# Optimization experiments

Measured on AMD Instinct MI355X. Metric: run time of the kernel, lower is better.

The kernel has to match this reference:

```python
import jax, jax.numpy as jnp
import numpy as np

B, N, D, H, DH, E, BIAS_DIM = 8, 512, 512, 8, 64, 32768, 8

def setup_inputs() -> dict:
    key = jax.random.key(0)
    ks = jax.random.split(key, 10)
    states = jax.random.normal(ks[0], (B, N, D), jnp.float32)
    key_states = jax.random.normal(ks[1], (B, N, D), jnp.float32)
    # causal mask, broadcastable over heads: [B,1,N,N]
    masks = jnp.broadcast_to(jnp.tril(jnp.ones((N, N), jnp.float32)), (B, 1, N, N))
    edge_type = jax.random.randint(ks[2], (E, 1), 0, BIAS_DIM, jnp.int32)
    b_idx = jax.random.randint(ks[3], (E, 1), 0, B, jnp.int32)
    q_idx = jax.random.randint(ks[4], (E, 1), 0, N, jnp.int32)
    k_idx = jax.random.randint(ks[5], (E, 1), 0, N, jnp.int32)
    attention_bias = jnp.concatenate([edge_type, b_idx, q_idx, k_idx], axis=1)
    s = 0.05
    Wq = jax.random.normal(ks[6], (D, H, DH), jnp.float32) * s
    Wk = jax.random.normal(ks[7], (D, H, DH), jnp.float32) * s
    Wv = jax.random.normal(ks[8], (D, H, DH), jnp.float32) * s
    k2 = jax.random.split(ks[9], 3)
    Wo = jax.random.normal(k2[0], (H, DH, D), jnp.float32) * s
    bias_embs = jax.random.normal(k2[1], (BIAS_DIM, DH), jnp.float32) * s
    bias_scalar = jax.random.normal(k2[2], (DH, 1), jnp.float32) * s
    return {"states": states, "key_states": key_states, "masks": masks,
            "attention_bias": attention_bias, "Wq": Wq, "Wk": Wk, "Wv": Wv,
            "Wo": Wo, "bias_embs": bias_embs, "bias_scalar": bias_scalar}

def reference(states, key_states, masks, attention_bias, Wq, Wk, Wv, Wo, bias_embs, bias_scalar):
    q = jnp.einsum('btd,dha->btha', states, Wq)
    k = jnp.einsum('btd,dha->btha', key_states, Wk)
    v = jnp.einsum('btd,dha->btha', key_states, Wv)
    alpha = jnp.einsum('bkha,bqha->bhqk', k, q)  # [B,H,Q,K]
    # sparse edge bias: embed edge types, project to scalar, scatter into [B,Q,K]
    et = attention_bias[:, 0]
    bias_vals = (bias_embs[et] @ bias_scalar)[:, 0]  # [E]
    bq, bk = alpha.shape[2], alpha.shape[3]
    bias_mat = jnp.zeros((alpha.shape[0], bq, bk), alpha.dtype)
    bias_mat = bias_mat.at[attention_bias[:, 1], attention_bias[:, 2], attention_bias[:, 3]].add(bias_vals)
    summed_keys = jnp.sum(k, axis=-1)  # [B,K,H]
    alpha = alpha + jnp.einsum('bqk,bkh->bhqk', bias_mat, summed_keys)
    alpha = alpha * jax.lax.rsqrt(jnp.float32(DH))
    neg = jnp.finfo(jnp.float32).min
    alpha = alpha * masks + (1.0 - jnp.ceil(masks)) * neg
    alpha = jax.nn.softmax(alpha, axis=-1)
    alpha = alpha * masks
    context = jnp.einsum('bhqk,bkha->bqha', alpha, v)
    return jnp.einsum('btha,had->btd', context, Wo)
```

## Files before the change

### kernel.cpp

```cpp
#include <hip/hip_runtime.h>

typedef unsigned short u16;
typedef unsigned int u32;
typedef __bf16 bf16x8 __attribute__((ext_vector_type(8)));
typedef float f32x4 __attribute__((ext_vector_type(4)));
typedef u16 u16x8 __attribute__((ext_vector_type(8)));
typedef u16 u16x4 __attribute__((ext_vector_type(4)));


__device__ __forceinline__ u16 f2b(float f) {
  union { float f; u32 i; } v; v.f = f;
  u32 r = v.i + 0x7fffu + ((v.i >> 16) & 1u);
  return (u16)(r >> 16);
}
__device__ __forceinline__ float b2f(u16 u) {
  union { u32 i; float f; } v; v.i = ((u32)u) << 16; return v.f;
}

__global__ __launch_bounds__(256) void prologue(
    const float* __restrict__ states, const float* __restrict__ key_states,
    const float* __restrict__ Wq, const float* __restrict__ Wk,
    const float* __restrict__ Wv, const float* __restrict__ Wo,
    const int* __restrict__ ab, const float* __restrict__ be,
    const float* __restrict__ bsc,
    u16* __restrict__ sb, u16* __restrict__ kbin, u16* __restrict__ wbase,
    float* __restrict__ bias_mat, int n_edges) {
  __shared__ u16 t[32][33];
  __shared__ float tv[8];
  int bid = blockIdx.x;
  int tid = threadIdx.x;
  if (bid < 2048) {
    const float* src = (bid >= 1024) ? key_states : states;
    u16* dst = (bid >= 1024) ? kbin : sb;
    int gid = (bid & 1023) * 256 + tid;
    const float4* sp = (const float4*)src + (size_t)gid * 2;
    float4 x0 = sp[0], x1 = sp[1];
    u16x8 p;
    p[0] = f2b(x0.x); p[1] = f2b(x0.y); p[2] = f2b(x0.z); p[3] = f2b(x0.w);
    p[4] = f2b(x1.x); p[5] = f2b(x1.y); p[6] = f2b(x1.z); p[7] = f2b(x1.w);
    *(u16x8*)(dst + (size_t)gid * 8) = p;
  } else if (bid < 3072) {
    int tt = bid - 2048;
    int z = tt >> 8, rem = tt & 255;
    int bx = rem & 15, by = rem >> 4;
    const float* src; float sc = 1.f;
    if (z == 0)      { src = Wq; sc = 0.125f; }
    else if (z == 1) { src = Wk; }
    else if (z == 2) { src = Wv; }
    else             { src = Wo; }
    u16* dst = wbase + (size_t)z * 262144;
    int tx = tid & 31, ty = tid >> 5;
    int c0 = bx * 32, r0 = by * 32;
    #pragma unroll
    for (int i = ty; i < 32; i += 8) t[i][tx] = f2b(src[(r0 + i) * 512 + c0 + tx] * sc);
    __syncthreads();
    #pragma unroll
    for (int i = ty; i < 32; i += 8) dst[(c0 + i) * 512 + r0 + tx] = t[tx][i];
  } else {
    if (tid < 8) {
      float s = 0.f;
      #pragma unroll
      for (int a = 0; a < 64; a++) s += be[tid * 64 + a] * bsc[a];
      tv[tid] = s * 0.125f;
    }
    __syncthreads();
    int e = (bid - 3072) * 256 + tid;
    if (e < n_edges) {
      int et = ab[e * 4 + 0];
      int b  = ab[e * 4 + 1];
      int qi = ab[e * 4 + 2];
      int ki = ab[e * 4 + 3];
      atomicAdd(&bias_mat[((size_t)b * 512 + qi) * 512 + ki], tv[et]);
    }
  }
}

__global__ __launch_bounds__(256) void qkv_gemm(const u16* __restrict__ sb,
                                                const u16* __restrict__ kbin,
                                                const u16* __restrict__ wT,
                                                u16* __restrict__ qb,
                                                u16* __restrict__ kbo,
                                                u16* __restrict__ vtb) {
  __shared__ u16 As[128 * 72];
  __shared__ u16 Bs[128 * 72];
  int tid = threadIdx.x;
  int lane = tid & 63, wave = tid >> 6;
  int quad = lane >> 4, ln = lane & 15;
  int wr = wave >> 1, wc = wave & 1;
  int row0 = blockIdx.x * 128;
  int col0 = blockIdx.y * 128;
  const u16* A = (col0 < 512) ? sb : kbin;
  int ar = tid >> 1;
  int ac = (tid & 1) * 32;

  f32x4 acc[4][4];
  #pragma unroll
  for (int i = 0; i < 4; i++)
    #pragma unroll
    for (int j = 0; j < 4; j++) acc[i][j] = (f32x4){0.f, 0.f, 0.f, 0.f};

  const u16* ap = A + (size_t)(row0 + ar) * 512 + ac;
  const u16* bp = wT + (size_t)(col0 + ar) * 512 + ac;

  u16x8 ra0, ra1, ra2, ra3, rb0, rb1, rb2, rb3;
  ra0 = *(const u16x8*)(ap + 0);  ra1 = *(const u16x8*)(ap + 8);
  ra2 = *(const u16x8*)(ap + 16); ra3 = *(const u16x8*)(ap + 24);
  rb0 = *(const u16x8*)(bp + 0);  rb1 = *(const u16x8*)(bp + 8);
  rb2 = *(const u16x8*)(bp + 16); rb3 = *(const u16x8*)(bp + 24);

  for (int k0 = 0; k0 < 512; k0 += 64) {
    __syncthreads();
    *(u16x8*)&As[ar * 72 + ac + 0]  = ra0;  *(u16x8*)&As[ar * 72 + ac + 8]  = ra1;
    *(u16x8*)&As[ar * 72 + ac + 16] = ra2;  *(u16x8*)&As[ar * 72 + ac + 24] = ra3;
    *(u16x8*)&Bs[ar * 72 + ac + 0]  = rb0;  *(u16x8*)&Bs[ar * 72 + ac + 8]  = rb1;
    *(u16x8*)&Bs[ar * 72 + ac + 16] = rb2;  *(u16x8*)&Bs[ar * 72 + ac + 24] = rb3;
    __syncthreads();
    if (k0 < 448) {
      int kn = k0 + 64;
      ra0 = *(const u16x8*)(ap + kn + 0);  ra1 = *(const u16x8*)(ap + kn + 8);
      ra2 = *(const u16x8*)(ap + kn + 16); ra3 = *(const u16x8*)(ap + kn + 24);
      rb0 = *(const u16x8*)(bp + kn + 0);  rb1 = *(const u16x8*)(bp + kn + 8);
      rb2 = *(const u16x8*)(bp + kn + 16); rb3 = *(const u16x8*)(bp + kn + 24);
    }
    #pragma unroll
    for (int s = 0; s < 2; s++) {
      bf16x8 af[4], bfv[4];
      #pragma unroll
      for (int i = 0; i < 4; i++)
        af[i] = *(bf16x8*)&As[(wr * 64 + i * 16 + ln) * 72 + s * 32 + quad * 8];
      #pragma unroll
      for (int j = 0; j < 4; j++)
        bfv[j] = *(bf16x8*)&Bs[(wc * 64 + j * 16 + ln) * 72 + s * 32 + quad * 8];
      #pragma unroll
      for (int i = 0; i < 4; i++)
        #pragma unroll
        for (int j = 0; j < 4; j++)
          acc[i][j] = __builtin_amdgcn_mfma_f32_16x16x32_bf16(af[i], bfv[j], acc[i][j], 0, 0, 0);
    }
  }

  int region = col0 >> 9;
  int nbase = col0 & 511;
  if (region <= 1) {
    u16* Cout = region ? kbo : qb;
    #pragma unroll
    for (int i = 0; i < 4; i++)
      #pragma unroll
      for (int j = 0; j < 4; j++) {
        int mb = row0 + wr * 64 + i * 16 + quad * 4;
        int n = nbase + wc * 64 + j * 16 + ln;
        #pragma unroll
        for (int r = 0; r < 4; r++)
          Cout[(size_t)(mb + r) * 512 + n] = f2b(acc[i][j][r]);
      }
  } else {
    #pragma unroll
    for (int i = 0; i < 4; i++)
      #pragma unroll
      for (int j = 0; j < 4; j++) {
        int mb = row0 + wr * 64 + i * 16 + quad * 4;
        int bb = mb >> 9, t0 = mb & 511;
        int a_abs = nbase + wc * 64 + j * 16 + ln;
        int h = a_abs >> 6, a = a_abs & 63;
        u16x4 p;
        p[0] = f2b(acc[i][j][0]); p[1] = f2b(acc[i][j][1]);
        p[2] = f2b(acc[i][j][2]); p[3] = f2b(acc[i][j][3]);
        *(u16x4*)&vtb[(((size_t)bb * 8 + h) * 64 + a) * 512 + t0] = p;
      }
  }
}

__global__ __launch_bounds__(256) void out_gemm(const u16* __restrict__ A,
                                                const u16* __restrict__ BT,
                                                float* __restrict__ C) {
  __shared__ u16 As[128 * 72];
  __shared__ u16 Bs[128 * 72];
  int tid = threadIdx.x;
  int lane = tid & 63, wave = tid >> 6;
  int quad = lane >> 4, ln = lane & 15;
  int wr = wave >> 1, wc = wave & 1;
  int row0 = blockIdx.x * 128;
  int col0 = blockIdx.y * 128;
  int ar = tid >> 1;
  int ac = (tid & 1) * 32;

  f32x4 acc[4][4];
  #pragma unroll
  for (int i = 0; i < 4; i++)
    #pragma unroll
    for (int j = 0; j < 4; j++) acc[i][j] = (f32x4){0.f, 0.f, 0.f, 0.f};

  const u16* ap = A + (size_t)(row0 + ar) * 512 + ac;
  const u16* bp = BT + (size_t)(col0 + ar) * 512 + ac;

  u16x8 ra0, ra1, ra2, ra3, rb0, rb1, rb2, rb3;
  ra0 = *(const u16x8*)(ap + 0);  ra1 = *(const u16x8*)(ap + 8);
  ra2 = *(const u16x8*)(ap + 16); ra3 = *(const u16x8*)(ap + 24);
  rb0 = *(const u16x8*)(bp + 0);  rb1 = *(const u16x8*)(bp + 8);
  rb2 = *(const u16x8*)(bp + 16); rb3 = *(const u16x8*)(bp + 24);

  for (int k0 = 0; k0 < 512; k0 += 64) {
    __syncthreads();
    *(u16x8*)&As[ar * 72 + ac + 0]  = ra0;  *(u16x8*)&As[ar * 72 + ac + 8]  = ra1;
    *(u16x8*)&As[ar * 72 + ac + 16] = ra2;  *(u16x8*)&As[ar * 72 + ac + 24] = ra3;
    *(u16x8*)&Bs[ar * 72 + ac + 0]  = rb0;  *(u16x8*)&Bs[ar * 72 + ac + 8]  = rb1;
    *(u16x8*)&Bs[ar * 72 + ac + 16] = rb2;  *(u16x8*)&Bs[ar * 72 + ac + 24] = rb3;
    __syncthreads();
    if (k0 < 448) {
      int kn = k0 + 64;
      ra0 = *(const u16x8*)(ap + kn + 0);  ra1 = *(const u16x8*)(ap + kn + 8);
      ra2 = *(const u16x8*)(ap + kn + 16); ra3 = *(const u16x8*)(ap + kn + 24);
      rb0 = *(const u16x8*)(bp + kn + 0);  rb1 = *(const u16x8*)(bp + kn + 8);
      rb2 = *(const u16x8*)(bp + kn + 16); rb3 = *(const u16x8*)(bp + kn + 24);
    }
    #pragma unroll
    for (int s = 0; s < 2; s++) {
      bf16x8 af[4], bfv[4];
      #pragma unroll
      for (int i = 0; i < 4; i++)
        af[i] = *(bf16x8*)&As[(wr * 64 + i * 16 + ln) * 72 + s * 32 + quad * 8];
      #pragma unroll
      for (int j = 0; j < 4; j++)
        bfv[j] = *(bf16x8*)&Bs[(wc * 64 + j * 16 + ln) * 72 + s * 32 + quad * 8];
      #pragma unroll
      for (int i = 0; i < 4; i++)
        #pragma unroll
        for (int j = 0; j < 4; j++)
          acc[i][j] = __builtin_amdgcn_mfma_f32_16x16x32_bf16(af[i], bfv[j], acc[i][j], 0, 0, 0);
    }
  }
  #pragma unroll
  for (int i = 0; i < 4; i++)
    #pragma unroll
    for (int j = 0; j < 4; j++) {
      int mb = row0 + wr * 64 + i * 16 + quad * 4;
      int n = col0 + wc * 64 + j * 16 + ln;
      #pragma unroll
      for (int r = 0; r < 4; r++)
        C[(size_t)(mb + r) * 512 + n] = acc[i][j][r];
    }
}

__global__ __launch_bounds__(256) void sumk2(const u16* __restrict__ k,
                                             float* __restrict__ summed) {
  int gid = blockIdx.x * 256 + threadIdx.x;
  int group = gid >> 3;
  int b = group >> 12, rem = group & 4095;
  int t = rem >> 3, h = rem & 7;
  int j = gid & 7;
  u16x8 x = *(const u16x8*)(k + ((size_t)(b * 512 + t)) * 512 + h * 64 + j * 8);
  float s = 0.f;
  #pragma unroll
  for (int e = 0; e < 8; e++) s += b2f(x[e]);
  s += __shfl_xor(s, 1);
  s += __shfl_xor(s, 2);
  s += __shfl_xor(s, 4);
  if (j == 0) summed[(b * 8 + h) * 512 + t] = s;
}

__global__ __launch_bounds__(256) void attn_mfma(const u16* __restrict__ q,
                                                 const u16* __restrict__ k,
                                                 const u16* __restrict__ vt,
                                                 const float* __restrict__ bias_mat,
                                                 const float* __restrict__ summed,
                                                 u16* __restrict__ ctx) {
  __shared__ u16 Qs[64 * 72];
  __shared__ u16 Ks[64 * 72];
  __shared__ u16 Vt[64 * 72];
  __shared__ u16 Ps[4][16 * 72];
  int tid = threadIdx.x;
  int wave = tid >> 6, lane = tid & 63;
  int quad = lane >> 4, ln = lane & 15;
  int blk = blockIdx.x;
  int p = blk & 3, bh = blk >> 2;
  int b = bh >> 3, h = bh & 7;

  int sr = tid >> 2;
  int sc2 = (tid & 3) * 16;

  const u16* kp0 = k + ((size_t)(b * 512 + sr)) * 512 + h * 64 + sc2;
  const u16* vp0 = vt + ((size_t)(bh * 64 + sr)) * 512 + sc2;

  #pragma unroll
  for (int ph = 0; ph < 2; ph++) {
    int qt = ph ? (7 - p) : p;
    int q0 = qt * 64;

    __syncthreads();
    {
      const u16* qp = q + ((size_t)(b * 512 + q0 + sr)) * 512 + h * 64 + sc2;
      *(u16x8*)&Qs[sr * 72 + sc2] = *(const u16x8*)qp;
      *(u16x8*)&Qs[sr * 72 + sc2 + 8] = *(const u16x8*)(qp + 8);
    }

    float m_r[4], l_r[4];
    f32x4 o[4];
    #pragma unroll
    for (int r = 0; r < 4; r++) { m_r[r] = -3.40282347e38f; l_r[r] = 0.f; }
    #pragma unroll
    for (int nt = 0; nt < 4; nt++) o[nt] = (f32x4){0.f, 0.f, 0.f, 0.f};

    u16x8 rk0 = *(const u16x8*)kp0;
    u16x8 rk1 = *(const u16x8*)(kp0 + 8);
    u16x8 rv0 = *(const u16x8*)vp0;
    u16x8 rv1 = *(const u16x8*)(vp0 + 8);

    for (int kb = 0; kb <= qt; kb++) {
      __syncthreads();
      *(u16x8*)&Ks[sr * 72 + sc2] = rk0;
      *(u16x8*)&Ks[sr * 72 + sc2 + 8] = rk1;
      *(u16x8*)&Vt[sr * 72 + sc2] = rv0;
      *(u16x8*)&Vt[sr * 72 + sc2 + 8] = rv1;
      __syncthreads();
      if (kb < qt) {
        const u16* kp = kp0 + (size_t)(kb + 1) * 64 * 512;
        const u16* vp = vp0 + (kb + 1) * 64;
        rk0 = *(const u16x8*)kp;
        rk1 = *(const u16x8*)(kp + 8);
        rv0 = *(const u16x8*)vp;
        rv1 = *(const u16x8*)(vp + 8);
      }

      int qrow = q0 + wave * 16 + quad * 4;
      float skv[4], bias_r[4][4];
      #pragma unroll
      for (int nt = 0; nt < 4; nt++) {
        int t = kb * 64 + nt * 16 + ln;
        skv[nt] = summed[bh * 512 + t];
        const float* bp = bias_mat + ((size_t)(b * 512 + qrow)) * 512 + t;
        #pragma unroll
        for (int r = 0; r < 4; r++) bias_r[nt][r] = bp[(size_t)r * 512];
      }

      bf16x8 aq0 = *(bf16x8*)&Qs[(wave * 16 + ln) * 72 + quad * 8];
      bf16x8 aq1 = *(bf16x8*)&Qs[(wave * 16 + ln) * 72 + 32 + quad * 8];
      f32x4 s[4];
      #pragma unroll
      for (int nt = 0; nt < 4; nt++) {
        bf16x8 b0 = *(bf16x8*)&Ks[(nt * 16 + ln) * 72 + quad * 8];
        bf16x8 b1 = *(bf16x8*)&Ks[(nt * 16 + ln) * 72 + 32 + quad * 8];
        s[nt] = (f32x4){0.f, 0.f, 0.f, 0.f};
        s[nt] = __builtin_amdgcn_mfma_f32_16x16x32_bf16(aq0, b0, s[nt], 0, 0, 0);
        s[nt] = __builtin_amdgcn_mfma_f32_16x16x32_bf16(aq1, b1, s[nt], 0, 0, 0);
      }

      #pragma unroll
      for (int nt = 0; nt < 4; nt++) {
        int t = kb * 64 + nt * 16 + ln;
        #pragma unroll
        for (int r = 0; r < 4; r++) {
          float val = s[nt][r] + bias_r[nt][r] * skv[nt];
          s[nt][r] = (t <= qrow + r) ? val : -3.40282347e38f;
        }
      }

      float alpha[4];
      #pragma unroll
      for (int r = 0; r < 4; r++) {
        float tm = fmaxf(fmaxf(s[0][r], s[1][r]), fmaxf(s[2][r], s[3][r]));
        #pragma unroll
        for (int off = 8; off; off >>= 1) tm = fmaxf(tm, __shfl_xor(tm, off));
        float mn = fmaxf(m_r[r], tm);
        alpha[r] = __expf(m_r[r] - mn);
        m_r[r] = mn;
        float rs = 0.f;
        #pragma unroll
        for (int nt = 0; nt < 4; nt++) {
          float pp = __expf(s[nt][r] - mn);
          s[nt][r] = pp;
          rs += pp;
        }
        #pragma unroll
        for (int off = 8; off; off >>= 1) rs += __shfl_xor(rs, off);
        l_r[r] = l_r[r] * alpha[r] + rs;
      }

      #pragma unroll
      for (int nt = 0; nt < 4; nt++)
        #pragma unroll
        for (int r = 0; r < 4; r++)
          Ps[wave][(quad * 4 + r) * 72 + nt * 16 + ln] = f2b(s[nt][r]);
      #pragma unroll
      for (int nt = 0; nt < 4; nt++)
        #pragma unroll
        for (int r = 0; r < 4; r++)
          o[nt][r] *= alpha[r];

      bf16x8 ap0 = *(bf16x8*)&Ps[wave][ln * 72 + quad * 8];
      bf16x8 ap1 = *(bf16x8*)&Ps[wave][ln * 72 + 32 + quad * 8];
      #pragma unroll
      for (int nt = 0; nt < 4; nt++) {
        bf16x8 b0 = *(bf16x8*)&Vt[(nt * 16 + ln) * 72 + quad * 8];
        bf16x8 b1 = *(bf16x8*)&Vt[(nt * 16 + ln) * 72 + 32 + quad * 8];
        o[nt] = __builtin_amdgcn_mfma_f32_16x16x32_bf16(ap0, b0, o[nt], 0, 0, 0);
        o[nt] = __builtin_amdgcn_mfma_f32_16x16x32_bf16(ap1, b1, o[nt], 0, 0, 0);
      }
    }

    #pragma unroll
    for (int r = 0; r < 4; r++) {
      float inv = 1.f / l_r[r];
      int qrow = q0 + wave * 16 + quad * 4 + r;
      u16* dst = ctx + ((size_t)(b * 512 + qrow)) * 512 + h * 64;
      #pragma unroll
      for (int nt = 0; nt < 4; nt++)
        dst[nt * 16 + ln] = f2b(o[nt][r] * inv);
    }
  }
}

extern "C" void kernel_launch(void* const* d_in, const int* in_sizes, int n_in,
                              void* d_out, int out_size, void* d_ws, size_t ws_size,
                              hipStream_t stream) {
  const float* states     = (const float*)d_in[0];
  const float* key_states = (const float*)d_in[1];
  const int*   ab         = (const int*)d_in[3];
  const float* Wq         = (const float*)d_in[4];
  const float* Wk         = (const float*)d_in[5];
  const float* Wv         = (const float*)d_in[6];
  const float* Wo         = (const float*)d_in[7];
  const float* be         = (const float*)d_in[8];
  const float* bsc        = (const float*)d_in[9];
  float* out = (float*)d_out;

  char* ws = (char*)d_ws;
  const size_t MB = 1024 * 1024;
  u16* wbase    = (u16*)(ws);
  u16* wot      = (u16*)(ws + 1536 * 1024);
  u16* sb       = (u16*)(ws + 2 * MB);
  u16* kbin     = (u16*)(ws + 6 * MB);
  u16* qb       = (u16*)(ws + 10 * MB);
  u16* kbo      = (u16*)(ws + 14 * MB);
  u16* vtb      = (u16*)(ws + 18 * MB);
  u16* ctxb     = (u16*)(ws + 22 * MB);
  float* bias_m = (float*)(ws + 26 * MB);
  float* summed = (float*)(ws + 34 * MB);

  int n_edges = in_sizes[3] / 4;

  hipMemsetAsync(bias_m, 0, (size_t)8 * MB, stream);
  prologue<<<dim3(3072 + (n_edges + 255) / 256), 256, 0, stream>>>(
      states, key_states, Wq, Wk, Wv, Wo, ab, be, bsc, sb, kbin, wbase, bias_m, n_edges);
  qkv_gemm<<<dim3(32, 12), 256, 0, stream>>>(sb, kbin, wbase, qb, kbo, vtb);
  sumk2<<<dim3(1024), 256, 0, stream>>>(kbo, summed);
  attn_mfma<<<dim3(256), 256, 0, stream>>>(qb, kbo, vtb, bias_m, summed, ctxb);
  out_gemm<<<dim3(32, 4), 256, 0, stream>>>(ctxb, wot, out);
}
```

Baseline: 150.9 us.

## Split long attention rows across blocks and shrink GEMM tiles for more parallelism

The attention kernel now launches 768 blocks instead of 256. Each block handles one query tile; query tiles 4-7 are split into two key ranges whose partial outputs and max/sum stats go to a workspace. A new merge kernel then combines them with log-sum-exp rescaling. This replaces the old balanced pairing of query tiles within one block. The bias and summed-key loads are now prefetched one key block ahead. The QKV and output GEMMs use smaller tiles (64x128 and 64x64) to raise block count on the many-CU device, at the cost of less data reuse, an extra kernel launch and extra fp32 partial traffic.

```diff
diff --git a/kernel.cpp b/kernel.cpp
--- a/kernel.cpp
+++ b/kernel.cpp
@@ -81,60 +81,56 @@
                                                 u16* __restrict__ qb,
                                                 u16* __restrict__ kbo,
                                                 u16* __restrict__ vtb) {
-  __shared__ u16 As[128 * 72];
+  __shared__ u16 As[64 * 72];
   __shared__ u16 Bs[128 * 72];
   int tid = threadIdx.x;
   int lane = tid & 63, wave = tid >> 6;
   int quad = lane >> 4, ln = lane & 15;
-  int wr = wave >> 1, wc = wave & 1;
-  int row0 = blockIdx.x * 128;
+  int row0 = blockIdx.x * 64;
   int col0 = blockIdx.y * 128;
   const u16* A = (col0 < 512) ? sb : kbin;
-  int ar = tid >> 1;
-  int ac = (tid & 1) * 32;
-
-  f32x4 acc[4][4];
+  int ara = tid >> 2, aca = (tid & 3) * 16;
+  int arb = tid >> 1, acb = (tid & 1) * 32;
+
+  f32x4 acc[4][2];
   #pragma unroll
   for (int i = 0; i < 4; i++)
     #pragma unroll
-    for (int j = 0; j < 4; j++) acc[i][j] = (f32x4){0.f, 0.f, 0.f, 0.f};
-
-  const u16* ap = A + (size_t)(row0 + ar) * 512 + ac;
-  const u16* bp = wT + (size_t)(col0 + ar) * 512 + ac;
-
-  u16x8 ra0, ra1, ra2, ra3, rb0, rb1, rb2, rb3;
+    for (int j = 0; j < 2; j++) acc[i][j] = (f32x4){0.f, 0.f, 0.f, 0.f};
+
+  const u16* ap = A + (size_t)(row0 + ara) * 512 + aca;
+  const u16* bp = wT + (size_t)(col0 + arb) * 512 + acb;
+
+  u16x8 ra0, ra1, rb0, rb1, rb2, rb3;
   ra0 = *(const u16x8*)(ap + 0);  ra1 = *(const u16x8*)(ap + 8);
-  ra2 = *(const u16x8*)(ap + 16); ra3 = *(const u16x8*)(ap + 24);
   rb0 = *(const u16x8*)(bp + 0);  rb1 = *(const u16x8*)(bp + 8);
   rb2 = *(const u16x8*)(bp + 16); rb3 = *(const u16x8*)(bp + 24);
 
   for (int k0 = 0; k0 < 512; k0 += 64) {
     __syncthreads();
-    *(u16x8*)&As[ar * 72 + ac + 0]  = ra0;  *(u16x8*)&As[ar * 72 + ac + 8]  = ra1;
-    *(u16x8*)&As[ar * 72 + ac + 16] = ra2;  *(u16x8*)&As[ar * 72 + ac + 24] = ra3;
-    *(u16x8*)&Bs[ar * 72 + ac + 0]  = rb0;  *(u16x8*)&Bs[ar * 72 + ac + 8]  = rb1;
-    *(u16x8*)&Bs[ar * 72 + ac + 16] = rb2;  *(u16x8*)&Bs[ar * 72 + ac + 24] = rb3;
+    *(u16x8*)&As[ara * 72 + aca + 0] = ra0;  *(u16x8*)&As[ara * 72 + aca + 8] = ra1;
+    *(u16x8*)&Bs[arb * 72 + acb + 0]  = rb0;  *(u16x8*)&Bs[arb * 72 + acb + 8]  = rb1;
+    *(u16x8*)&Bs[arb * 72 + acb + 16] = rb2;  *(u16x8*)&Bs[arb * 72 + acb + 24] = rb3;
     __syncthreads();
     if (k0 < 448) {
       int kn = k0 + 64;
       ra0 = *(const u16x8*)(ap + kn + 0);  ra1 = *(const u16x8*)(ap + kn + 8);
-      ra2 = *(const u16x8*)(ap + kn + 16); ra3 = *(const u16x8*)(ap + kn + 24);
       rb0 = *(const u16x8*)(bp + kn + 0);  rb1 = *(const u16x8*)(bp + kn + 8);
       rb2 = *(const u16x8*)(bp + kn + 16); rb3 = *(const u16x8*)(bp + kn + 24);
     }
     #pragma unroll
     for (int s = 0; s < 2; s++) {
-      bf16x8 af[4], bfv[4];
+      bf16x8 af[4], bfv[2];
       #pragma unroll
       for (int i = 0; i < 4; i++)
-        af[i] = *(bf16x8*)&As[(wr * 64 + i * 16 + ln) * 72 + s * 32 + quad * 8];
-      #pragma unroll
-      for (int j = 0; j < 4; j++)
-        bfv[j] = *(bf16x8*)&Bs[(wc * 64 + j * 16 + ln) * 72 + s * 32 + quad * 8];
+        af[i] = *(bf16x8*)&As[(i * 16 + ln) * 72 + s * 32 + quad * 8];
+      #pragma unroll
+      for (int j = 0; j < 2; j++)
+        bfv[j] = *(bf16x8*)&Bs[(wave * 32 + j * 16 + ln) * 72 + s * 32 + quad * 8];
       #pragma unroll
       for (int i = 0; i < 4; i++)
         #pragma unroll
-        for (int j = 0; j < 4; j++)
+        for (int j = 0; j < 2; j++)
           acc[i][j] = __builtin_amdgcn_mfma_f32_16x16x32_bf16(af[i], bfv[j], acc[i][j], 0, 0, 0);
     }
   }
@@ -146,9 +142,9 @@
     #pragma unroll
     for (int i = 0; i < 4; i++)
       #pragma unroll
-      for (int j = 0; j < 4; j++) {
-        int mb = row0 + wr * 64 + i * 16 + quad * 4;
-        int n = nbase + wc * 64 + j * 16 + ln;
+      for (int j = 0; j < 2; j++) {
+        int mb = row0 + i * 16 + quad * 4;
+        int n = nbase + wave * 32 + j * 16 + ln;
         #pragma unroll
         for (int r = 0; r < 4; r++)
           Cout[(size_t)(mb + r) * 512 + n] = f2b(acc[i][j][r]);
@@ -157,10 +153,10 @@
     #pragma unroll
     for (int i = 0; i < 4; i++)
       #pragma unroll
-      for (int j = 0; j < 4; j++) {
-        int mb = row0 + wr * 64 + i * 16 + quad * 4;
+      for (int j = 0; j < 2; j++) {
+        int mb = row0 + i * 16 + quad * 4;
         int bb = mb >> 9, t0 = mb & 511;
-        int a_abs = nbase + wc * 64 + j * 16 + ln;
+        int a_abs = nbase + wave * 32 + j * 16 + ln;
         int h = a_abs >> 6, a = a_abs & 63;
         u16x4 p;
         p[0] = f2b(acc[i][j][0]); p[1] = f2b(acc[i][j][1]);
@@ -173,68 +169,61 @@
 __global__ __launch_bounds__(256) void out_gemm(const u16* __restrict__ A,
                                                 const u16* __restrict__ BT,
                                                 float* __restrict__ C) {
-  __shared__ u16 As[128 * 72];
-  __shared__ u16 Bs[128 * 72];
+  __shared__ u16 As[64 * 72];
+  __shared__ u16 Bs[64 * 72];
   int tid = threadIdx.x;
   int lane = tid & 63, wave = tid >> 6;
   int quad = lane >> 4, ln = lane & 15;
   int wr = wave >> 1, wc = wave & 1;
-  int row0 = blockIdx.x * 128;
-  int col0 = blockIdx.y * 128;
-  int ar = tid >> 1;
-  int ac = (tid & 1) * 32;
-
-  f32x4 acc[4][4];
-  #pragma unroll
-  for (int i = 0; i < 4; i++)
-    #pragma unroll
-    for (int j = 0; j < 4; j++) acc[i][j] = (f32x4){0.f, 0.f, 0.f, 0.f};
+  int row0 = blockIdx.x * 64;
+  int col0 = blockIdx.y * 64;
+  int ar = tid >> 2, ac = (tid & 3) * 16;
+
+  f32x4 acc[2][2];
+  #pragma unroll
+  for (int i = 0; i < 2; i++)
+    #pragma unroll
+    for (int j = 0; j < 2; j++) acc[i][j] = (f32x4){0.f, 0.f, 0.f, 0.f};
 
   const u16* ap = A + (size_t)(row0 + ar) * 512 + ac;
   const u16* bp = BT + (size_t)(col0 + ar) * 512 + ac;
 
-  u16x8 ra0, ra1, ra2, ra3, rb0, rb1, rb2, rb3;
-  ra0 = *(const u16x8*)(ap + 0);  ra1 = *(const u16x8*)(ap + 8);
-  ra2 = *(const u16x8*)(ap + 16); ra3 = *(const u16x8*)(ap + 24);
-  rb0 = *(const u16x8*)(bp + 0);  rb1 = *(const u16x8*)(bp + 8);
-  rb2 = *(const u16x8*)(bp + 16); rb3 = *(const u16x8*)(bp + 24);
+  u16x8 ra0, ra1, rb0, rb1;
+  ra0 = *(const u16x8*)(ap + 0); ra1 = *(const u16x8*)(ap + 8);
+  rb0 = *(const u16x8*)(bp + 0); rb1 = *(const u16x8*)(bp + 8);
 
   for (int k0 = 0; k0 < 512; k0 += 64) {
     __syncthreads();
-    *(u16x8*)&As[ar * 72 + ac + 0]  = ra0;  *(u16x8*)&As[ar * 72 + ac + 8]  = ra1;
-    *(u16x8*)&As[ar * 72 + ac + 16] = ra2;  *(u16x8*)&As[ar * 72 + ac + 24] = ra3;
-    *(u16x8*)&Bs[ar * 72 + ac + 0]  = rb0;  *(u16x8*)&Bs[ar * 72 + ac + 8]  = rb1;
-    *(u16x8*)&Bs[ar * 72 + ac + 16] = rb2;  *(u16x8*)&Bs[ar * 72 + ac + 24] = rb3;
+    *(u16x8*)&As[ar * 72 + ac + 0] = ra0;  *(u16x8*)&As[ar * 72 + ac + 8] = ra1;
+    *(u16x8*)&Bs[ar * 72 + ac + 0] = rb0;  *(u16x8*)&Bs[ar * 72 + ac + 8] = rb1;
     __syncthreads();
     if (k0 < 448) {
       int kn = k0 + 64;
-      ra0 = *(const u16x8*)(ap + kn + 0);  ra1 = *(const u16x8*)(ap + kn + 8);
-      ra2 = *(const u16x8*)(ap + kn + 16); ra3 = *(const u16x8*)(ap + kn + 24);
-      rb0 = *(const u16x8*)(bp + kn + 0);  rb1 = *(const u16x8*)(bp + kn + 8);
-      rb2 = *(const u16x8*)(bp + kn + 16); rb3 = *(const u16x8*)(bp + kn + 24);
+      ra0 = *(const u16x8*)(ap + kn + 0); ra1 = *(const u16x8*)(ap + kn + 8);
+      rb0 = *(const u16x8*)(bp + kn + 0); rb1 = *(const u16x8*)(bp + kn + 8);
     }
     #pragma unroll
     for (int s = 0; s < 2; s++) {
-      bf16x8 af[4], bfv[4];
-      #pragma unroll
-      for (int i = 0; i < 4; i++)
-        af[i] = *(bf16x8*)&As[(wr * 64 + i * 16 + ln) * 72 + s * 32 + quad * 8];
-      #pragma unroll
-      for (int j = 0; j < 4; j++)
-        bfv[j] = *(bf16x8*)&Bs[(wc * 64 + j * 16 + ln) * 72 + s * 32 + quad * 8];
-      #pragma unroll
-      for (int i = 0; i < 4; i++)
+      bf16x8 af[2], bfv[2];
+      #pragma unroll
+      for (int i = 0; i < 2; i++)
+        af[i] = *(bf16x8*)&As[(wr * 32 + i * 16 + ln) * 72 + s * 32 + quad * 8];
+      #pragma unroll
+      for (int j = 0; j < 2; j++)
+        bfv[j] = *(bf16x8*)&Bs[(wc * 32 + j * 16 + ln) * 72 + s * 32 + quad * 8];
+      #pragma unroll
+      for (int i = 0; i < 2; i++)
         #pragma unroll
-        for (int j = 0; j < 4; j++)
+        for (int j = 0; j < 2; j++)
           acc[i][j] = __builtin_amdgcn_mfma_f32_16x16x32_bf16(af[i], bfv[j], acc[i][j], 0, 0, 0);
     }
   }
   #pragma unroll
-  for (int i = 0; i < 4; i++)
-    #pragma unroll
-    for (int j = 0; j < 4; j++) {
-      int mb = row0 + wr * 64 + i * 16 + quad * 4;
-      int n = col0 + wc * 64 + j * 16 + ln;
+  for (int i = 0; i < 2; i++)
+    #pragma unroll
+    for (int j = 0; j < 2; j++) {
+      int mb = row0 + wr * 32 + i * 16 + quad * 4;
+      int n = col0 + wc * 32 + j * 16 + ln;
       #pragma unroll
       for (int r = 0; r < 4; r++)
         C[(size_t)(mb + r) * 512 + n] = acc[i][j][r];
@@ -263,7 +252,9 @@
                                                  const u16* __restrict__ vt,
                                                  const float* __restrict__ bias_mat,
                                                  const float* __restrict__ summed,
-                                                 u16* __restrict__ ctx) {
+                                                 u16* __restrict__ ctx,
+                                                 float* __restrict__ Opart,
+                                                 float* __restrict__ ml) {
   __shared__ u16 Qs[64 * 72];
   __shared__ u16 Ks[64 * 72];
   __shared__ u16 Vt[64 * 72];
@@ -272,141 +263,203 @@
   int wave = tid >> 6, lane = tid & 63;
   int quad = lane >> 4, ln = lane & 15;
   int blk = blockIdx.x;
-  int p = blk & 3, bh = blk >> 2;
+  int bh = blk / 12;
+  int u = blk - bh * 12;
   int b = bh >> 3, h = bh & 7;
+  int qt, kb0, kbe, part = 0;
+  bool partial;
+  if (u < 4) { qt = u; kb0 = 0; kbe = u; partial = false; }
+  else {
+    int v = u - 4; qt = 4 + (v >> 1); part = v & 1; partial = true;
+    if (part == 0) { kb0 = 0; kbe = 3; } else { kb0 = 4; kbe = qt; }
+  }
+  int q0 = qt * 64;
 
   int sr = tid >> 2;
   int sc2 = (tid & 3) * 16;
 
+  {
+    const u16* qp = q + ((size_t)(b * 512 + q0 + sr)) * 512 + h * 64 + sc2;
+    *(u16x8*)&Qs[sr * 72 + sc2] = *(const u16x8*)qp;
+    *(u16x8*)&Qs[sr * 72 + sc2 + 8] = *(const u16x8*)(qp + 8);
+  }
+
+  float m_r[4], l_r[4];
+  f32x4 o[4];
+  #pragma unroll
+  for (int r = 0; r < 4; r++) { m_r[r] = -3.40282347e38f; l_r[r] = 0.f; }
+  #pragma unroll
+  for (int nt = 0; nt < 4; nt++) o[nt] = (f32x4){0.f, 0.f, 0.f, 0.f};
+
   const u16* kp0 = k + ((size_t)(b * 512 + sr)) * 512 + h * 64 + sc2;
   const u16* vp0 = vt + ((size_t)(bh * 64 + sr)) * 512 + sc2;
 
-  #pragma unroll
-  for (int ph = 0; ph < 2; ph++) {
-    int qt = ph ? (7 - p) : p;
-    int q0 = qt * 64;
-
-    __syncthreads();
-    {
-      const u16* qp = q + ((size_t)(b * 512 + q0 + sr)) * 512 + h * 64 + sc2;
-      *(u16x8*)&Qs[sr * 72 + sc2] = *(const u16x8*)qp;
-      *(u16x8*)&Qs[sr * 72 + sc2 + 8] = *(const u16x8*)(qp + 8);
-    }
-
-    float m_r[4], l_r[4];
-    f32x4 o[4];
-    #pragma unroll
-    for (int r = 0; r < 4; r++) { m_r[r] = -3.40282347e38f; l_r[r] = 0.f; }
-    #pragma unroll
-    for (int nt = 0; nt < 4; nt++) o[nt] = (f32x4){0.f, 0.f, 0.f, 0.f};
-
-    u16x8 rk0 = *(const u16x8*)kp0;
-    u16x8 rk1 = *(const u16x8*)(kp0 + 8);
-    u16x8 rv0 = *(const u16x8*)vp0;
-    u16x8 rv1 = *(const u16x8*)(vp0 + 8);
-
-    for (int kb = 0; kb <= qt; kb++) {
-      __syncthreads();
-      *(u16x8*)&Ks[sr * 72 + sc2] = rk0;
-      *(u16x8*)&Ks[sr * 72 + sc2 + 8] = rk1;
-      *(u16x8*)&Vt[sr * 72 + sc2] = rv0;
-      *(u16x8*)&Vt[sr * 72 + sc2 + 8] = rv1;
-      __syncthreads();
-      if (kb < qt) {
-        const u16* kp = kp0 + (size_t)(kb + 1) * 64 * 512;
-        const u16* vp = vp0 + (kb + 1) * 64;
-        rk0 = *(const u16x8*)kp;
-        rk1 = *(const u16x8*)(kp + 8);
-        rv0 = *(const u16x8*)vp;
-        rv1 = *(const u16x8*)(vp + 8);
-      }
-
-      int qrow = q0 + wave * 16 + quad * 4;
-      float skv[4], bias_r[4][4];
+  u16x8 rk0 = *(const u16x8*)(kp0 + (size_t)kb0 * 64 * 512);
+  u16x8 rk1 = *(const u16x8*)(kp0 + (size_t)kb0 * 64 * 512 + 8);
+  u16x8 rv0 = *(const u16x8*)(vp0 + kb0 * 64);
+  u16x8 rv1 = *(const u16x8*)(vp0 + kb0 * 64 + 8);
+
+  int qrow = q0 + wave * 16 + quad * 4;
+
+  float c_skv[4], c_bias[4][4];
+  #pragma unroll
+  for (int nt = 0; nt < 4; nt++) {
+    int t = kb0 * 64 + nt * 16 + ln;
+    c_skv[nt] = summed[bh * 512 + t];
+    const float* bp2 = bias_mat + ((size_t)(b * 512 + qrow)) * 512 + t;
+    #pragma unroll
+    for (int r = 0; r < 4; r++) c_bias[nt][r] = bp2[(size_t)r * 512];
+  }
+
+  for (int kb = kb0; kb <= kbe; kb++) {
+    __syncthreads();
+    *(u16x8*)&Ks[sr * 72 + sc2] = rk0;
+    *(u16x8*)&Ks[sr * 72 + sc2 + 8] = rk1;
+    *(u16x8*)&Vt[sr * 72 + sc2] = rv0;
+    *(u16x8*)&Vt[sr * 72 + sc2 + 8] = rv1;
+    __syncthreads();
+
+    float n_skv[4], n_bias[4][4];
+    if (kb < kbe) {
+      const u16* kp = kp0 + (size_t)(kb + 1) * 64 * 512;
+      const u16* vp = vp0 + (kb + 1) * 64;
+      rk0 = *(const u16x8*)kp;
+      rk1 = *(const u16x8*)(kp + 8);
+      rv0 = *(const u16x8*)vp;
+      rv1 = *(const u16x8*)(vp + 8);
       #pragma unroll
       for (int nt = 0; nt < 4; nt++) {
-        int t = kb * 64 + nt * 16 + ln;
-        skv[nt] = summed[bh * 512 + t];
-        const float* bp = bias_mat + ((size_t)(b * 512 + qrow)) * 512 + t;
+        int t = (kb + 1) * 64 + nt * 16 + ln;
+        n_skv[nt] = summed[bh * 512 + t];
+        const float* bp2 = bias_mat + ((size_t)(b * 512 + qrow)) * 512 + t;
         #pragma unroll
-        for (int r = 0; r < 4; r++) bias_r[nt][r] = bp[(size_t)r * 512];
-      }
-
-      bf16x8 aq0 = *(bf16x8*)&Qs[(wave * 16 + ln) * 72 + quad * 8];
-      bf16x8 aq1 = *(bf16x8*)&Qs[(wave * 16 + ln) * 72 + 32 + quad * 8];
-      f32x4 s[4];
+        for (int r = 0; r < 4; r++) n_bias[nt][r] = bp2[(size_t)r * 512];
+      }
+    }
+
+    bf16x8 aq0 = *(bf16x8*)&Qs[(wave * 16 + ln) * 72 + quad * 8];
+    bf16x8 aq1 = *(bf16x8*)&Qs[(wave * 16 + ln) * 72 + 32 + quad * 8];
+    f32x4 s[4];
+    #pragma unroll
+    for (int nt = 0; nt < 4; nt++) {
+      bf16x8 b0 = *(bf16x8*)&Ks[(nt * 16 + ln) * 72 + quad * 8];
+      bf16x8 b1 = *(bf16x8*)&Ks[(nt * 16 + ln) * 72 + 32 + quad * 8];
+      s[nt] = (f32x4){0.f, 0.f, 0.f, 0.f};
+      s[nt] = __builtin_amdgcn_mfma_f32_16x16x32_bf16(aq0, b0, s[nt], 0, 0, 0);
+      s[nt] = __builtin_amdgcn_mfma_f32_16x16x32_bf16(aq1, b1, s[nt], 0, 0, 0);
+    }
+
+    #pragma unroll
+    for (int nt = 0; nt < 4; nt++) {
+      int t = kb * 64 + nt * 16 + ln;
+      #pragma unroll
+      for (int r = 0; r < 4; r++) {
+        float val = s[nt][r] + c_bias[nt][r] * c_skv[nt];
+        s[nt][r] = (t <= qrow + r) ? val : -3.40282347e38f;
+      }
+    }
+
+    float alpha[4];
+    #pragma unroll
+    for (int r = 0; r < 4; r++) {
+      float tm = fmaxf(fmaxf(s[0][r], s[1][r]), fmaxf(s[2][r], s[3][r]));
+      #pragma unroll
+      for (int off = 8; off; off >>= 1) tm = fmaxf(tm, __shfl_xor(tm, off));
+      float mn = fmaxf(m_r[r], tm);
+      alpha[r] = __expf(m_r[r] - mn);
+      m_r[r] = mn;
+      float rs = 0.f;
       #pragma unroll
       for (int nt = 0; nt < 4; nt++) {
-        bf16x8 b0 = *(bf16x8*)&Ks[(nt * 16 + ln) * 72 + quad * 8];
-        bf16x8 b1 = *(bf16x8*)&Ks[(nt * 16 + ln) * 72 + 32 + quad * 8];
-        s[nt] = (f32x4){0.f, 0.f, 0.f, 0.f};
-        s[nt] = __builtin_amdgcn_mfma_f32_16x16x32_bf16(aq0, b0, s[nt], 0, 0, 0);
-        s[nt] = __builtin_amdgcn_mfma_f32_16x16x32_bf16(aq1, b1, s[nt], 0, 0, 0);
-      }
-
+        float pp = __expf(s[nt][r] - mn);
+        s[nt][r] = pp;
+        rs += pp;
+      }
+      #pragma unroll
+      for (int off = 8; off; off >>= 1) rs += __shfl_xor(rs, off);
+      l_r[r] = l_r[r] * alpha[r] + rs;
+    }
+
+    #pragma unroll
+    for (int nt = 0; nt < 4; nt++)
+      #pragma unroll
+      for (int r = 0; r < 4; r++)
+        Ps[wave][(quad * 4 + r) * 72 + nt * 16 + ln] = f2b(s[nt][r]);
+    #pragma unroll
+    for (int nt = 0; nt < 4; nt++)
+      #pragma unroll
+      for (int r = 0; r < 4; r++)
+        o[nt][r] *= alpha[r];
+
+    bf16x8 ap0 = *(bf16x8*)&Ps[wave][ln * 72 + quad * 8];
+    bf16x8 ap1 = *(bf16x8*)&Ps[wave][ln * 72 + 32 + quad * 8];
+    #pragma unroll
+    for (int nt = 0; nt < 4; nt++) {
+      bf16x8 b0 = *(bf16x8*)&Vt[(nt * 16 + ln) * 72 + quad * 8];
+      bf16x8 b1 = *(bf16x8*)&Vt[(nt * 16 + ln) * 72 + 32 + quad * 8];
+      o[nt] = __builtin_amdgcn_mfma_f32_16x16x32_bf16(ap0, b0, o[nt], 0, 0, 0);
+      o[nt] = __builtin_amdgcn_mfma_f32_16x16x32_bf16(ap1, b1, o[nt], 0, 0, 0);
+    }
+
+    if (kb < kbe) {
       #pragma unroll
       for (int nt = 0; nt < 4; nt++) {
-        int t = kb * 64 + nt * 16 + ln;
+        c_skv[nt] = n_skv[nt];
         #pragma unroll
-        for (int r = 0; r < 4; r++) {
-          float val = s[nt][r] + bias_r[nt][r] * skv[nt];
-          s[nt][r] = (t <= qrow + r) ? val : -3.40282347e38f;
-        }
-      }
-
-      float alpha[4];
-      #pragma unroll
-      for (int r = 0; r < 4; r++) {
-        float tm = fmaxf(fmaxf(s[0][r], s[1][r]), fmaxf(s[2][r], s[3][r]));
-        #pragma unroll
-        for (int off = 8; off; off >>= 1) tm = fmaxf(tm, __shfl_xor(tm, off));
-        float mn = fmaxf(m_r[r], tm);
-        alpha[r] = __expf(m_r[r] - mn);
-        m_r[r] = mn;
-        float rs = 0.f;
-        #pragma unroll
-        for (int nt = 0; nt < 4; nt++) {
-          float pp = __expf(s[nt][r] - mn);
-          s[nt][r] = pp;
-          rs += pp;
-        }
-        #pragma unroll
-        for (int off = 8; off; off >>= 1) rs += __shfl_xor(rs, off);
-        l_r[r] = l_r[r] * alpha[r] + rs;
-      }
-
-      #pragma unroll
-      for (int nt = 0; nt < 4; nt++)
-        #pragma unroll
-        for (int r = 0; r < 4; r++)
-          Ps[wave][(quad * 4 + r) * 72 + nt * 16 + ln] = f2b(s[nt][r]);
-      #pragma unroll
-      for (int nt = 0; nt < 4; nt++)
-        #pragma unroll
-        for (int r = 0; r < 4; r++)
-          o[nt][r] *= alpha[r];
-
-      bf16x8 ap0 = *(bf16x8*)&Ps[wave][ln * 72 + quad * 8];
-      bf16x8 ap1 = *(bf16x8*)&Ps[wave][ln * 72 + 32 + quad * 8];
-      #pragma unroll
-      for (int nt = 0; nt < 4; nt++) {
-        bf16x8 b0 = *(bf16x8*)&Vt[(nt * 16 + ln) * 72 + quad * 8];
-        bf16x8 b1 = *(bf16x8*)&Vt[(nt * 16 + ln) * 72 + 32 + quad * 8];
-        o[nt] = __builtin_amdgcn_mfma_f32_16x16x32_bf16(ap0, b0, o[nt], 0, 0, 0);
-        o[nt] = __builtin_amdgcn_mfma_f32_16x16x32_bf16(ap1, b1, o[nt], 0, 0, 0);
-      }
-    }
-
+        for (int r = 0; r < 4; r++) c_bias[nt][r] = n_bias[nt][r];
+      }
+    }
+  }
+
+  if (!partial) {
     #pragma unroll
     for (int r = 0; r < 4; r++) {
       float inv = 1.f / l_r[r];
-      int qrow = q0 + wave * 16 + quad * 4 + r;
-      u16* dst = ctx + ((size_t)(b * 512 + qrow)) * 512 + h * 64;
+      int qr2 = qrow + r;
+      u16* dst = ctx + ((size_t)(b * 512 + qr2)) * 512 + h * 64;
       #pragma unroll
       for (int nt = 0; nt < 4; nt++)
         dst[nt * 16 + ln] = f2b(o[nt][r] * inv);
     }
-  }
+  } else {
+    #pragma unroll
+    for (int r = 0; r < 4; r++) {
+      int row = qrow + r - 256;
+      float* dst = Opart + (((size_t)(part * 64 + bh)) * 256 + row) * 64;
+      #pragma unroll
+      for (int nt = 0; nt < 4; nt++)
+        dst[nt * 16 + ln] = o[nt][r];
+    }
+    if (ln == 0) {
+      #pragma unroll
+      for (int r = 0; r < 4; r++) {
+        int row = qrow + r - 256;
+        float* mp = ml + (((size_t)(part * 64 + bh)) * 256 + row) * 2;
+        mp[0] = m_r[r];
+        mp[1] = l_r[r];
+      }
+    }
+  }
+}
+
+__global__ __launch_bounds__(256) void attn_merge(const float* __restrict__ Opart,
+                                                  const float* __restrict__ ml,
+                                                  u16* __restrict__ ctx) {
+  int gid = blockIdx.x * 256 + threadIdx.x;
+  int col = gid & 63;
+  int row = (gid >> 6) & 255;
+  int bh = gid >> 14;
+  size_t i0 = (size_t)bh * 256 + row;
+  size_t i1 = (size_t)(64 + bh) * 256 + row;
+  float m0 = ml[i0 * 2], l0 = ml[i0 * 2 + 1];
+  float m1 = ml[i1 * 2], l1 = ml[i1 * 2 + 1];
+  float m = fmaxf(m0, m1);
+  float a0 = __expf(m0 - m), a1 = __expf(m1 - m);
+  float l = l0 * a0 + l1 * a1;
+  float O0 = Opart[i0 * 64 + col], O1 = Opart[i1 * 64 + col];
+  float val = (O0 * a0 + O1 * a1) / l;
+  int b = bh >> 3, h = bh & 7, qrow = 256 + row;
+  ctx[((size_t)(b * 512 + qrow)) * 512 + h * 64 + col] = f2b(val);
 }
 
 extern "C" void kernel_launch(void* const* d_in, const int* in_sizes, int n_in,
@@ -435,14 +488,17 @@
   u16* ctxb     = (u16*)(ws + 22 * MB);
   float* bias_m = (float*)(ws + 26 * MB);
   float* summed = (float*)(ws + 34 * MB);
+  float* Opart  = (float*)(ws + 35 * MB);
+  float* mlbuf  = (float*)(ws + 43 * MB);
 
   int n_edges = in_sizes[3] / 4;
 
   hipMemsetAsync(bias_m, 0, (size_t)8 * MB, stream);
   prologue<<<dim3(3072 + (n_edges + 255) / 256), 256, 0, stream>>>(
       states, key_states, Wq, Wk, Wv, Wo, ab, be, bsc, sb, kbin, wbase, bias_m, n_edges);
-  qkv_gemm<<<dim3(32, 12), 256, 0, stream>>>(sb, kbin, wbase, qb, kbo, vtb);
+  qkv_gemm<<<dim3(64, 12), 256, 0, stream>>>(sb, kbin, wbase, qb, kbo, vtb);
   sumk2<<<dim3(1024), 256, 0, stream>>>(kbo, summed);
-  attn_mfma<<<dim3(256), 256, 0, stream>>>(qb, kbo, vtb, bias_m, summed, ctxb);
-  out_gemm<<<dim3(32, 4), 256, 0, stream>>>(ctxb, wot, out);
-}
+  attn_mfma<<<dim3(768), 256, 0, stream>>>(qb, kbo, vtb, bias_m, summed, ctxb, Opart, mlbuf);
+  attn_merge<<<dim3(4096), 256, 0, stream>>>(Opart, mlbuf, ctxb);
+  out_gemm<<<dim3(64, 8), 256, 0, stream>>>(ctxb, wot, out);
+}
```

New measurement: 139.3 us. -7.7%, faster.
